# Kernel optimization log

Hardware: AMD Instinct MI355X
Metric: run time of the kernel (lower is better)

## Reference

```python
import jax, jax.numpy as jnp
import numpy as np

EPS = 1e-10


def setup_inputs() -> dict:
    key = jax.random.key(0)
    kx, ky = jax.random.split(key)
    x = jax.random.normal(kx, (8, 8192, 3), dtype=jnp.float32)
    y = jax.random.normal(ky, (8, 8192, 3), dtype=jnp.float32)
    return {"x": x, "y": y}


def reference(x, y):
    # x: (B, N, 3), y: (B, M, 3)
    xy = -2.0 * jnp.einsum("bnd,bmd->bnm", x, y)          # (B, N, M)
    xx = jnp.sum(x * x, axis=-1, keepdims=True)            # (B, N, 1)
    yy = jnp.sum(y * y, axis=-1, keepdims=True)            # (B, M, 1)
    dist = jnp.sqrt(xy + xx + jnp.swapaxes(yy, 1, 2) + EPS)  # (B, N, M)
    distance1 = jnp.min(dist, axis=2)                      # (B, N): x -> nearest y
    distance2 = jnp.min(dist, axis=1)                      # (B, M): y -> nearest x
    mean1 = jnp.mean(distance1, axis=-1)                   # (B,)
    mean2 = jnp.mean(distance2, axis=-1)                   # (B,)
    return jnp.sum(jnp.maximum(mean1, mean2))
```

## Files before the change

### kernel.cpp

```cpp
#include <hip/hip_runtime.h>


#define BB 8
#define NN 8192
#define NPTS (BB*NN)
#define BLK 256
#define CCOLS 256
#define CT 8
#define RT 4
#define STRIPS 16

typedef __attribute__((ext_vector_type(8))) short bf16x8;
typedef __attribute__((ext_vector_type(16))) float f32x16;

__device__ __forceinline__ unsigned f2mono(float f) {
    unsigned u = __float_as_uint(f);
    return u ^ ((unsigned)((int)u >> 31) | 0x80000000u);
}
__device__ __forceinline__ float mono2f(unsigned m) {
    unsigned u = ((int)m >= 0) ? ~m : (m ^ 0x80000000u);
    return __uint_as_float(u);
}
__device__ __forceinline__ unsigned bfh(float v) {
    unsigned u = __float_as_uint(v);
    u += 0x7FFFu + ((u >> 16) & 1u);
    return u >> 16;
}
__device__ __forceinline__ float bff(unsigned h) {
    return __uint_as_float(h << 16);
}
__device__ __forceinline__ unsigned pk(unsigned lo, unsigned hi) {
    return (lo & 0xFFFFu) | (hi << 16);
}

__global__ void prep_kernel(const float* __restrict__ x, const float* __restrict__ y,
                            uint4* __restrict__ afr, uint4* __restrict__ bfr,
                            unsigned* __restrict__ counter) {
    int i = blockIdx.x * BLK + threadIdx.x;
    if (i == 0) *counter = 0;
    const float* src = (i < NPTS) ? x : y;
    int j = (i < NPTS) ? i : i - NPTS;
    float c0 = src[3*j], c1 = src[3*j+1], c2 = src[3*j+2];
    float s2 = c0*c0 + c1*c1 + c2*c2;
    unsigned sh = bfh(s2), sl = bfh(s2 - bff(sh));
    float a0 = -2.f*c0, a1 = -2.f*c1, a2 = -2.f*c2;
    unsigned ah0 = bfh(a0), ah1 = bfh(a1), ah2 = bfh(a2);
    unsigned al0 = bfh(a0 - bff(ah0)), al1 = bfh(a1 - bff(ah1)), al2 = bfh(a2 - bff(ah2));
    unsigned bh0 = bfh(c0), bh1 = bfh(c1), bh2 = bfh(c2);
    unsigned bl0 = bfh(c0 - bff(bh0)), bl1 = bfh(c1 - bff(bh1)), bl2 = bfh(c2 - bff(bh2));
    const unsigned one = 0x3F80u;
    afr[2*i]   = make_uint4(pk(ah0,ah1), pk(ah2,al0), pk(al1,al2), pk(ah0,ah1));
    afr[2*i+1] = make_uint4(pk(ah2,sh),  pk(sl,one),  pk(one,0u),  0u);
    bfr[2*i]   = make_uint4(pk(bh0,bh1), pk(bh2,bh0), pk(bh1,bh2), pk(bl0,bl1));
    bfr[2*i+1] = make_uint4(pk(bl2,one), pk(one,sh),  pk(sl,0u),   0u);
}

__device__ __forceinline__ bf16x8 cvt(uint4 v) { return __builtin_bit_cast(bf16x8, v); }

__global__ __launch_bounds__(BLK, 2) void
main_kernel(const uint4* __restrict__ afr, const uint4* __restrict__ bfr,
            float* __restrict__ bpart, unsigned* __restrict__ counter,
            float* __restrict__ out) {
    __shared__ unsigned colmin[CCOLS];
    __shared__ float red[4];
    __shared__ float gg[8];
    __shared__ int lastflag;
    const int bi  = blockIdx.x;
    const int dir = bi >> 8;
    const int b   = (bi >> 5) & 7;
    const int cc  = bi & 31;
    const uint4* Af = afr + (dir ? 2*NPTS : 0);
    const uint4* Bf = bfr + (dir ? 0 : 2*NPTS);
    const int tid = threadIdx.x;
    const int lane = tid & 63, w = tid >> 6;
    const int m = lane & 31;
    const int hb = lane >> 5;

    colmin[tid] = 0xFFFFFFFFu;

    bf16x8 bf[CT];
#pragma unroll
    for (int ct = 0; ct < CT; ++ct) {
        int c = b * NN + cc * CCOLS + ct * 32 + m;
        bf[ct] = cvt(Bf[2*c + hb]);
    }

    f32x16 zro;
#pragma unroll
    for (int i = 0; i < 16; ++i) zro[i] = 0.f;

    float rm[CT];
#pragma unroll
    for (int ct = 0; ct < CT; ++ct) rm[ct] = 3.4e38f;

    const int rowbase = b * NN + w * 128 + m;
    uint4 cur[RT], nxt[RT];
#pragma unroll
    for (int t = 0; t < RT; ++t) cur[t] = Af[2*(rowbase + t*32) + hb];

#pragma unroll 1
    for (int s = 0; s < STRIPS; ++s) {
        const int np = (s + 1 < STRIPS) ? (s + 1) : s;
#pragma unroll
        for (int t = 0; t < RT; ++t) nxt[t] = Af[2*(rowbase + np*512 + t*32) + hb];
#pragma unroll
        for (int ct = 0; ct < CT; ++ct) {
            f32x16 a0 = __builtin_amdgcn_mfma_f32_32x32x16_bf16(cvt(cur[0]), bf[ct], zro, 0, 0, 0);
            f32x16 a1 = __builtin_amdgcn_mfma_f32_32x32x16_bf16(cvt(cur[1]), bf[ct], zro, 0, 0, 0);
            f32x16 a2 = __builtin_amdgcn_mfma_f32_32x32x16_bf16(cvt(cur[2]), bf[ct], zro, 0, 0, 0);
            f32x16 a3 = __builtin_amdgcn_mfma_f32_32x32x16_bf16(cvt(cur[3]), bf[ct], zro, 0, 0, 0);
            float p = rm[ct];
#pragma unroll
            for (int r = 0; r < 16; ++r) {
                float t0 = fminf(fminf(a0[r], a1[r]), a2[r]);
                p = fminf(fminf(t0, a3[r]), p);
            }
            rm[ct] = p;
        }
#pragma unroll
        for (int t = 0; t < RT; ++t) cur[t] = nxt[t];
    }

#pragma unroll
    for (int ct = 0; ct < CT; ++ct) {
        float p = fminf(rm[ct], __shfl_xor(rm[ct], 32, 64));
        if (hb == 0) atomicMin(&colmin[ct * 32 + m], f2mono(p));
    }
    __syncthreads();

    float d = sqrtf(fmaxf(mono2f(colmin[tid]), 0.f) + 1e-10f);
#pragma unroll
    for (int off = 32; off; off >>= 1) d += __shfl_down(d, off, 64);
    if (lane == 0) red[w] = d;
    __syncthreads();
    if (tid == 0) {
        float total = red[0] + red[1] + red[2] + red[3];
        atomicExch(&bpart[bi], total);
        __threadfence();
        unsigned old = atomicAdd(counter, 1u);
        lastflag = (old == 511u);
    }
    __syncthreads();

    if (lastflag) {
        float v0 = atomicAdd(&bpart[tid], 0.f);
        float v1 = atomicAdd(&bpart[256 + tid], 0.f);
#pragma unroll
        for (int off = 16; off; off >>= 1) {
            v0 += __shfl_down(v0, off, 32);
            v1 += __shfl_down(v1, off, 32);
        }
        if ((tid & 31) == 0) gg[tid >> 5] = fmaxf(v0, v1);
        __syncthreads();
        if (tid == 0) {
            float acc = 0.f;
#pragma unroll
            for (int k = 0; k < 8; ++k) acc += gg[k];
            out[0] = acc * (1.0f / (float)NN);
        }
    }
}

extern "C" void kernel_launch(void* const* d_in, const int* in_sizes, int n_in,
                              void* d_out, int out_size, void* d_ws, size_t ws_size,
                              hipStream_t stream) {
    const float* x = (const float*)d_in[0];
    const float* y = (const float*)d_in[1];
    float* out = (float*)d_out;

    char* ws = (char*)d_ws;
    uint4* afr = (uint4*)ws;
    uint4* bfr = afr + 4 * NPTS;
    float* bpart = (float*)(bfr + 4 * NPTS);
    unsigned* counter = (unsigned*)(bpart + 512);

    prep_kernel<<<(2 * NPTS) / BLK, BLK, 0, stream>>>(x, y, afr, bfr, counter);
    main_kernel<<<512, BLK, 0, stream>>>(afr, bfr, bpart, counter, out);
}
```

Measured before the change: 102.0 us.

## Halve column tile per block, double grid, and split min-reduction chains

Halves the column tile per block (CT 8→4, 128 columns) and doubles the grid to 1024 blocks, raising launch bounds to 4 waves-per-SIMD occupancy. The final cross-block reduction is rewritten to match the new block-to-(dir,batch) mapping. The fmin reduction over MFMA outputs is split into four independent accumulator chains and processes MFMA results in pairs to reduce register pressure and dependency latency. The cost is that each row strip is now reloaded by twice as many blocks, which doubles A-fragment traffic.

Result: slower. 111.3 us (+9.1%).

```diff
diff --git a/kernel.cpp b/kernel.cpp
--- a/kernel.cpp
+++ b/kernel.cpp
@@ -5,10 +5,11 @@
 #define NN 8192
 #define NPTS (BB*NN)
 #define BLK 256
-#define CCOLS 256
-#define CT 8
+#define CCOLS 128
+#define CT 4
 #define RT 4
 #define STRIPS 16
+#define GRID 1024
 
 typedef __attribute__((ext_vector_type(8))) short bf16x8;
 typedef __attribute__((ext_vector_type(16))) float f32x16;
@@ -57,18 +58,18 @@
 
 __device__ __forceinline__ bf16x8 cvt(uint4 v) { return __builtin_bit_cast(bf16x8, v); }
 
-__global__ __launch_bounds__(BLK, 2) void
+__global__ __launch_bounds__(BLK, 4) void
 main_kernel(const uint4* __restrict__ afr, const uint4* __restrict__ bfr,
             float* __restrict__ bpart, unsigned* __restrict__ counter,
             float* __restrict__ out) {
     __shared__ unsigned colmin[CCOLS];
     __shared__ float red[4];
-    __shared__ float gg[8];
+    __shared__ float gg[16];
     __shared__ int lastflag;
     const int bi  = blockIdx.x;
-    const int dir = bi >> 8;
-    const int b   = (bi >> 5) & 7;
-    const int cc  = bi & 31;
+    const int dir = bi >> 9;
+    const int b   = (bi >> 6) & 7;
+    const int cc  = bi & 63;
     const uint4* Af = afr + (dir ? 2*NPTS : 0);
     const uint4* Bf = bfr + (dir ? 0 : 2*NPTS);
     const int tid = threadIdx.x;
@@ -76,7 +77,7 @@
     const int m = lane & 31;
     const int hb = lane >> 5;
 
-    colmin[tid] = 0xFFFFFFFFu;
+    if (tid < CCOLS) colmin[tid] = 0xFFFFFFFFu;
 
     bf16x8 bf[CT];
 #pragma unroll
@@ -105,17 +106,30 @@
         for (int t = 0; t < RT; ++t) nxt[t] = Af[2*(rowbase + np*512 + t*32) + hb];
 #pragma unroll
         for (int ct = 0; ct < CT; ++ct) {
-            f32x16 a0 = __builtin_amdgcn_mfma_f32_32x32x16_bf16(cvt(cur[0]), bf[ct], zro, 0, 0, 0);
-            f32x16 a1 = __builtin_amdgcn_mfma_f32_32x32x16_bf16(cvt(cur[1]), bf[ct], zro, 0, 0, 0);
-            f32x16 a2 = __builtin_amdgcn_mfma_f32_32x32x16_bf16(cvt(cur[2]), bf[ct], zro, 0, 0, 0);
-            f32x16 a3 = __builtin_amdgcn_mfma_f32_32x32x16_bf16(cvt(cur[3]), bf[ct], zro, 0, 0, 0);
-            float p = rm[ct];
+            float p0 = rm[ct], p1 = 3.4e38f, p2 = 3.4e38f, p3 = 3.4e38f;
+            {
+                f32x16 a0 = __builtin_amdgcn_mfma_f32_32x32x16_bf16(cvt(cur[0]), bf[ct], zro, 0, 0, 0);
+                f32x16 a1 = __builtin_amdgcn_mfma_f32_32x32x16_bf16(cvt(cur[1]), bf[ct], zro, 0, 0, 0);
 #pragma unroll
-            for (int r = 0; r < 16; ++r) {
-                float t0 = fminf(fminf(a0[r], a1[r]), a2[r]);
-                p = fminf(fminf(t0, a3[r]), p);
+                for (int r = 0; r < 16; r += 4) {
+                    p0 = fminf(fminf(a0[r],   a1[r]),   p0);
+                    p1 = fminf(fminf(a0[r+1], a1[r+1]), p1);
+                    p2 = fminf(fminf(a0[r+2], a1[r+2]), p2);
+                    p3 = fminf(fminf(a0[r+3], a1[r+3]), p3);
+                }
             }
-            rm[ct] = p;
+            {
+                f32x16 a2 = __builtin_amdgcn_mfma_f32_32x32x16_bf16(cvt(cur[2]), bf[ct], zro, 0, 0, 0);
+                f32x16 a3 = __builtin_amdgcn_mfma_f32_32x32x16_bf16(cvt(cur[3]), bf[ct], zro, 0, 0, 0);
+#pragma unroll
+                for (int r = 0; r < 16; r += 4) {
+                    p0 = fminf(fminf(a2[r],   a3[r]),   p0);
+                    p1 = fminf(fminf(a2[r+1], a3[r+1]), p1);
+                    p2 = fminf(fminf(a2[r+2], a3[r+2]), p2);
+                    p3 = fminf(fminf(a2[r+3], a3[r+3]), p3);
+                }
+            }
+            rm[ct] = fminf(fminf(p0, p1), fminf(p2, p3));
         }
 #pragma unroll
         for (int t = 0; t < RT; ++t) cur[t] = nxt[t];
@@ -128,7 +142,8 @@
     }
     __syncthreads();
 
-    float d = sqrtf(fmaxf(mono2f(colmin[tid]), 0.f) + 1e-10f);
+    float d = 0.f;
+    if (tid < CCOLS) d = sqrtf(fmaxf(mono2f(colmin[tid]), 0.f) + 1e-10f);
 #pragma unroll
     for (int off = 32; off; off >>= 1) d += __shfl_down(d, off, 64);
     if (lane == 0) red[w] = d;
@@ -138,24 +153,24 @@
         atomicExch(&bpart[bi], total);
         __threadfence();
         unsigned old = atomicAdd(counter, 1u);
-        lastflag = (old == 511u);
+        lastflag = (old == GRID - 1);
     }
     __syncthreads();
 
     if (lastflag) {
-        float v0 = atomicAdd(&bpart[tid], 0.f);
-        float v1 = atomicAdd(&bpart[256 + tid], 0.f);
+        const int g = tid >> 4, k = tid & 15;
+        float v = 0.f;
 #pragma unroll
-        for (int off = 16; off; off >>= 1) {
-            v0 += __shfl_down(v0, off, 32);
-            v1 += __shfl_down(v1, off, 32);
-        }
-        if ((tid & 31) == 0) gg[tid >> 5] = fmaxf(v0, v1);
+        for (int j = 0; j < 4; ++j)
+            v += atomicAdd(&bpart[g * 64 + k * 4 + j], 0.f);
+#pragma unroll
+        for (int off = 8; off; off >>= 1) v += __shfl_down(v, off, 16);
+        if (k == 0) gg[g] = v;
         __syncthreads();
         if (tid == 0) {
             float acc = 0.f;
 #pragma unroll
-            for (int k = 0; k < 8; ++k) acc += gg[k];
+            for (int bb = 0; bb < BB; ++bb) acc += fmaxf(gg[bb], gg[BB + bb]);
             out[0] = acc * (1.0f / (float)NN);
         }
     }
@@ -172,8 +187,8 @@
     uint4* afr = (uint4*)ws;
     uint4* bfr = afr + 4 * NPTS;
     float* bpart = (float*)(bfr + 4 * NPTS);
-    unsigned* counter = (unsigned*)(bpart + 512);
+    unsigned* counter = (unsigned*)(bpart + GRID);
 
     prep_kernel<<<(2 * NPTS) / BLK, BLK, 0, stream>>>(x, y, afr, bfr, counter);
-    main_kernel<<<512, BLK, 0, stream>>>(afr, bfr, bpart, counter, out);
+    main_kernel<<<GRID, BLK, 0, stream>>>(afr, bfr, bpart, counter, out);
 }
```
